# Kernel tuning notes

Measured on AMD Instinct MI355X. Metric: run time of the kernel, lower is better.

The kernel has to match this reference:

```python
import jax, jax.numpy as jnp
import numpy as np

BN_EPS = 1e-5
K2 = 9  # 3x3 kernel


def _conv3x3(x, w, b):
    # x: [B,C,H,W], w: [O,C,3,3] -> [B,O,H,W], stride 1, pad 1
    out = jax.lax.conv_general_dilated(
        x, w, window_strides=(1, 1), padding=((1, 1), (1, 1)),
        dimension_numbers=("NCHW", "OIHW", "NCHW"))
    return out + b[None, :, None, None]


def setup_inputs() -> dict:
    key = jax.random.key(0)
    ks = jax.random.split(key, 8)
    B, C, H, W = 8, 256, 64, 64
    O = 256
    x = jax.random.normal(ks[0], (B, C, H, W), dtype=jnp.float32)
    # offset/mask conv: small init so sampled offsets stay near the base grid
    w_off = jax.random.normal(ks[1], (3 * K2, C, 3, 3), dtype=jnp.float32) * 0.01
    b_off = jnp.zeros((3 * K2,), dtype=jnp.float32)
    weight = jax.random.normal(ks[2], (O, C, 3, 3), dtype=jnp.float32) * 0.02
    bias = jnp.zeros((O,), dtype=jnp.float32)
    gamma = jnp.ones((O,), dtype=jnp.float32)
    beta = jnp.zeros((O,), dtype=jnp.float32)
    run_mean = jax.random.normal(ks[3], (O,), dtype=jnp.float32) * 0.1
    run_var = jax.random.uniform(ks[4], (O,), dtype=jnp.float32) + 0.5
    return {"x": x, "w_off": w_off, "b_off": b_off, "weight": weight,
            "bias": bias, "gamma": gamma, "beta": beta,
            "run_mean": run_mean, "run_var": run_var}


def _deform_sample(img, py, px):
    # img: [C,H,W]; py, px: [K2,H,W] sampling coordinates.
    # Bilinear sample with zero padding outside (DCNv2 semantics:
    # out-of-bounds corners contribute zero).
    C, H, W = img.shape
    y0 = jnp.floor(py)
    x0 = jnp.floor(px)
    wy1 = py - y0  # frac weights for the 'high' corner
    wx1 = px - x0

    def gather(yi, xi):
        valid = (yi >= 0) & (yi < H) & (xi >= 0) & (xi < W)
        yc = jnp.clip(yi, 0, H - 1).astype(jnp.int32)
        xc = jnp.clip(xi, 0, W - 1).astype(jnp.int32)
        return img[:, yc, xc] * valid.astype(img.dtype)[None]  # [C,K2,H,W]

    v00 = gather(y0, x0)
    v01 = gather(y0, x0 + 1)
    v10 = gather(y0 + 1, x0)
    v11 = gather(y0 + 1, x0 + 1)
    return (v00 * ((1 - wy1) * (1 - wx1))[None]
            + v01 * ((1 - wy1) * wx1)[None]
            + v10 * (wy1 * (1 - wx1))[None]
            + v11 * (wy1 * wx1)[None])  # [C,K2,H,W]


def reference(x, w_off, b_off, weight, bias, gamma, beta, run_mean, run_var):
    B, C, H, W = x.shape
    O = weight.shape[0]
    # 1) offset / mask branch (standard 3x3 conv)
    om = _conv3x3(x, w_off, b_off)  # [B, 27, H, W]
    off_y = om[:, :K2]
    off_x = om[:, K2:2 * K2]
    mask = jax.nn.sigmoid(om[:, 2 * K2:])  # modulation, [B,9,H,W]
    # 2) base sampling grid for 3x3, stride 1, pad 1, dilation 1
    ky = jnp.repeat(jnp.arange(3), 3).astype(x.dtype)  # [9]
    kx = jnp.tile(jnp.arange(3), 3).astype(x.dtype)    # [9]
    hs = jnp.arange(H, dtype=x.dtype)
    ws = jnp.arange(W, dtype=x.dtype)
    base_y = hs[None, :, None] - 1.0 + ky[:, None, None]  # [9,H,1]
    base_x = ws[None, None, :] - 1.0 + kx[:, None, None]  # [9,1,W]
    py = base_y[None] + off_y  # [B,9,H,W]
    px = base_x[None] + off_x
    # 3) modulated deformable im2col (bilinear gather) per batch
    cols = jax.vmap(_deform_sample)(x, py, px)  # [B,C,9,H,W]
    cols = cols * mask[:, None]                 # apply modulation mask
    # 4) GEMM over (C, K2) + bias
    w3 = weight.reshape(O, C, K2)
    out = jnp.einsum("ock,bckhw->bohw", w3, cols) + bias[None, :, None, None]
    # 5) BatchNorm (eval mode, running stats) + ReLU
    inv = gamma / jnp.sqrt(run_var + BN_EPS)
    out = out * inv[None, :, None, None] + (beta - run_mean * inv)[None, :, None, None]
    return jax.nn.relu(out)
```

## Files before the change

kernel.cpp:

```cpp
#include <hip/hip_runtime.h>
#include <math.h>

#define H 64
#define W 64
#define C 256
#define O 256
#define CK 2304
#define NB 8
#define HWSZ 4096

typedef __attribute__((ext_vector_type(8))) short short8;
typedef __attribute__((ext_vector_type(4))) float floatx4;
typedef __attribute__((ext_vector_type(4))) unsigned uintx4;

#define FSWZ(n) ((((n) & 3) << 1) | (((n) >> 2) & 1))

__device__ __forceinline__ float lo2f(unsigned u) {
  return __builtin_bit_cast(float, u << 16);
}
__device__ __forceinline__ float hi2f(unsigned u) {
  return __builtin_bit_cast(float, u & 0xffff0000u);
}
__device__ __forceinline__ unsigned pk2bf(float v0, float v1) {
  unsigned a = __builtin_bit_cast(unsigned, v0);
  unsigned b = __builtin_bit_cast(unsigned, v1);
  return ((a + 0x8000u) >> 16) | ((b + 0x8000u) & 0xffff0000u);
}

__global__ __launch_bounds__(256) void prep_all(
    const float* __restrict__ x, const float* __restrict__ weight,
    const float* __restrict__ w_off, const float* __restrict__ bias,
    const float* __restrict__ gamma, const float* __restrict__ beta,
    const float* __restrict__ run_mean, const float* __restrict__ run_var,
    unsigned short* __restrict__ xt, unsigned short* __restrict__ wb,
    unsigned short* __restrict__ wob, float* __restrict__ invsh) {
  __shared__ unsigned tile[64 * 65];
  int bid = blockIdx.x;
  int tid = threadIdx.x;

  if (bid < 1024) {
    int b = bid & 7;
    int t = bid >> 3;
    int y = t >> 1;
    int cg = t & 1;
    const float* xb = x + ((size_t)b * C + cg * 128) * HWSZ + y * W;
#pragma unroll
    for (int it = 0; it < 4; ++it) {
      int e = tid + 256 * it;
      int xx4 = e & 15;
      int cp = e >> 4;
      floatx4 f0 = *reinterpret_cast<const floatx4*>(
          xb + (size_t)(2 * cp) * HWSZ + xx4 * 4);
      floatx4 f1 = *reinterpret_cast<const floatx4*>(
          xb + (size_t)(2 * cp + 1) * HWSZ + xx4 * 4);
#pragma unroll
      for (int k = 0; k < 4; ++k)
        tile[cp * 65 + xx4 * 4 + k] = pk2bf(f0[k], f1[k]);
    }
    __syncthreads();
    unsigned short* xo = xt + ((size_t)(b * 64 + y) << 14) + cg * 128;
#pragma unroll
    for (int it = 0; it < 4; ++it) {
      int e = tid + 256 * it;
      int cq = e & 15;
      int xx = e >> 4;
      unsigned u0 = tile[(cq * 4 + 0) * 65 + xx];
      unsigned u1 = tile[(cq * 4 + 1) * 65 + xx];
      unsigned u2 = tile[(cq * 4 + 2) * 65 + xx];
      unsigned u3 = tile[(cq * 4 + 3) * 65 + xx];
      uint4 v = {u0, u1, u2, u3};
      *reinterpret_cast<uint4*>(xo + (xx << 8) + (cq << 3)) = v;
    }
  } else if (bid < 1312) {
    int d0 = ((bid - 1024) * 256 + tid) * 8;
    int lane = (d0 >> 3) & 63;
    int mt = (d0 >> 9) & 15;
    int ks = d0 >> 13;
    int o = mt * 16 + (lane & 15);
    int kn0 = ks * 32 + (lane >> 4) * 8;
    int tap = kn0 >> 8;
    int c0 = kn0 & 255;
    const float* wsrc = weight + o * CK + c0 * 9 + tap;
    unsigned pk[4];
#pragma unroll
    for (int p = 0; p < 4; ++p)
      pk[p] = pk2bf(wsrc[(2 * p) * 9], wsrc[(2 * p + 1) * 9]);
    uint4 v = {pk[0], pk[1], pk[2], pk[3]};
    *reinterpret_cast<uint4*>(wb + d0) = v;
  } else if (bid < 1348) {
    int d0 = ((bid - 1312) * 256 + tid) * 8;
    int lane = (d0 >> 3) & 63;
    int mt = (d0 >> 9) & 1;
    int ks = d0 >> 10;
    int o = mt * 16 + (lane & 15);
    int kn0 = ks * 32 + (lane >> 4) * 8;
    int tap = kn0 >> 8;
    int c0 = kn0 & 255;
    uint4 v;
    if (o < 27) {
      const float* wsrc = w_off + o * CK + c0 * 9 + tap;
      unsigned pk[4];
#pragma unroll
      for (int p = 0; p < 4; ++p)
        pk[p] = pk2bf(wsrc[(2 * p) * 9], wsrc[(2 * p + 1) * 9]);
      v = (uint4){pk[0], pk[1], pk[2], pk[3]};
    } else {
      v = (uint4){0, 0, 0, 0};
    }
    *reinterpret_cast<uint4*>(wob + d0) = v;
  } else {
    int o = tid;
    float inv = gamma[o] * rsqrtf(run_var[o] + 1e-5f);
    invsh[o] = inv;
    invsh[O + o] = beta[o] + (bias[o] - run_mean[o]) * inv;
  }
}

__device__ __forceinline__ void sample_tap(
    int tap, const unsigned short* __restrict__ xtb, short* __restrict__ colbuf,
    const int* __restrict__ sbase, const float* __restrict__ s00,
    const float* __restrict__ s01, const float* __restrict__ s10,
    const float* __restrict__ s11, int sn, int scb) {
  int ei = tap * 64 + sn;
  int base = sbase[ei];
  float w00 = s00[ei], w01 = s01[ei], w10 = s10[ei], w11 = s11[ei];
  const unsigned short* p = xtb + base;
#pragma unroll
  for (int i = 0; i < 4; ++i) {
    int cbw = (i << 3) | scb;
    int co = cbw << 3;
    uintx4 u00 = *reinterpret_cast<const uintx4*>(p + co);
    uintx4 u01 = *reinterpret_cast<const uintx4*>(p + 256 + co);
    uintx4 u10 = *reinterpret_cast<const uintx4*>(p + 16384 + co);
    uintx4 u11 = *reinterpret_cast<const uintx4*>(p + 16640 + co);
    uintx4 res;
#pragma unroll
    for (int jd = 0; jd < 4; ++jd) {
      float v0 = fmaf(w00, lo2f(u00[jd]),
                 fmaf(w01, lo2f(u01[jd]),
                 fmaf(w10, lo2f(u10[jd]), w11 * lo2f(u11[jd]))));
      float v1 = fmaf(w00, hi2f(u00[jd]),
                 fmaf(w01, hi2f(u01[jd]),
                 fmaf(w10, hi2f(u10[jd]), w11 * hi2f(u11[jd]))));
      res[jd] = pk2bf(v0, v1);
    }
    int pos = (cbw ^ FSWZ(sn)) & 31;
    *reinterpret_cast<uintx4*>(&colbuf[(sn << 8) + (pos << 3)]) = res;
  }
}

__device__ __forceinline__ void mfma_tap(
    int tap, const unsigned short* __restrict__ wb,
    const short* __restrict__ colbuf, int wvid, int lane, int q, int lm,
    floatx4 (&acc)[2][4]) {
  __builtin_amdgcn_s_setprio(1);
#pragma unroll
  for (int s = 0; s < 8; ++s) {
    int ks = tap * 8 + s;
    short8 afrag[2];
#pragma unroll
    for (int a = 0; a < 2; ++a)
      afrag[a] = *reinterpret_cast<const short8*>(
          wb + (((ks * 16 + wvid * 2 + a) * 64 + lane) << 3));
    short8 bfrag[4];
#pragma unroll
    for (int u = 0; u < 4; ++u) {
      int nn = u * 16 + lm;
      int pos = ((s * 4 + q) ^ FSWZ(nn)) & 31;
      bfrag[u] = *reinterpret_cast<const short8*>(&colbuf[(nn << 8) + (pos << 3)]);
    }
#pragma unroll
    for (int a = 0; a < 2; ++a)
#pragma unroll
      for (int u = 0; u < 4; ++u)
        acc[a][u] = __builtin_amdgcn_mfma_f32_16x16x32_bf16(
            afrag[a], bfrag[u], acc[a][u], 0, 0, 0);
  }
  __builtin_amdgcn_s_setprio(0);
}

__global__ __launch_bounds__(512, 4) void deform_mfma_kernel(
    const unsigned short* __restrict__ xt, const unsigned short* __restrict__ wob,
    const float* __restrict__ b_off, const unsigned short* __restrict__ wb,
    const float* __restrict__ invsh, float* __restrict__ out) {
  __shared__ short cols[2][64 * 256];
  __shared__ int sbase[576];
  __shared__ float s00[576], s01[576], s10[576], s11[576];
  float* sm_om = reinterpret_cast<float*>(&cols[0][0]);

  int tid = threadIdx.x;
  int lane = tid & 63;
  int wvid = tid >> 6;
  int q = lane >> 4;
  int lm = lane & 15;
  int b = blockIdx.x;
  int h = blockIdx.y;
  const unsigned short* xtb = xt + ((size_t)b << 20);

  {
    int mt = wvid & 1;
    int nq = wvid >> 1;
    floatx4 a0 = (floatx4){0.f, 0.f, 0.f, 0.f};
    int pxn = nq * 16 + lm;
    for (int tap = 0; tap < 9; ++tap) {
      int yy = h - 1 + tap / 3;
      int xx = pxn - 1 + tap % 3;
      bool vv = (yy >= 0) && (yy < H) && (xx >= 0) && (xx < W);
      const unsigned short* bp =
          xtb + ((((yy & 63) << 6) + (xx & 63)) << 8) + q * 8;
#pragma unroll
      for (int s = 0; s < 8; ++s) {
        int ks = tap * 8 + s;
        short8 afrag = *reinterpret_cast<const short8*>(
            wob + (((ks * 2 + mt) * 64 + lane) << 3));
        short8 bfrag;
        if (vv)
          bfrag = *reinterpret_cast<const short8*>(bp + s * 32);
        else
          bfrag = (short8){0, 0, 0, 0, 0, 0, 0, 0};
        a0 = __builtin_amdgcn_mfma_f32_16x16x32_bf16(afrag, bfrag, a0, 0, 0, 0);
      }
    }
#pragma unroll
    for (int r = 0; r < 4; ++r) {
      int o = mt * 16 + q * 4 + r;
      if (o < 27) sm_om[o * 64 + pxn] = a0[r] + b_off[o];
    }
  }
  __syncthreads();

  for (int e = tid; e < 576; e += 512) {
    int n = e & 63;
    int k = e >> 6;
    float oy = sm_om[k * 64 + n];
    float ox = sm_om[(9 + k) * 64 + n];
    float mv = sm_om[(18 + k) * 64 + n];
    float m = 1.0f / (1.0f + __expf(-mv));
    float py = (float)(h - 1 + k / 3) + oy;
    float px = (float)(n - 1 + k % 3) + ox;
    float yf = floorf(py), xf = floorf(px);
    int y0 = (int)yf, x0 = (int)xf;
    float fy = py - yf, fx = px - xf;
    float r0, r1; int yl;
    if (y0 >= 0 && y0 <= H - 2)      { yl = y0;    r0 = 1.f - fy; r1 = fy;       }
    else if (y0 == -1)               { yl = 0;     r0 = fy;       r1 = 0.f;      }
    else if (y0 == H - 1)            { yl = H - 2; r0 = 0.f;      r1 = 1.f - fy; }
    else                             { yl = 0;     r0 = 0.f;      r1 = 0.f;      }
    float c0, c1; int xl;
    if (x0 >= 0 && x0 <= W - 2)      { xl = x0;    c0 = 1.f - fx; c1 = fx;       }
    else if (x0 == -1)               { xl = 0;     c0 = fx;       c1 = 0.f;      }
    else if (x0 == W - 1)            { xl = W - 2; c0 = 0.f;      c1 = 1.f - fx; }
    else                             { xl = 0;     c0 = 0.f;      c1 = 0.f;      }
    r0 *= m; r1 *= m;
    sbase[e] = ((yl << 6) + xl) << 8;
    s00[e] = r0 * c0; s01[e] = r0 * c1;
    s10[e] = r1 * c0; s11[e] = r1 * c1;
  }
  __syncthreads();

  floatx4 acc[2][4];
#pragma unroll
  for (int a = 0; a < 2; ++a)
#pragma unroll
    for (int u = 0; u < 4; ++u) acc[a][u] = (floatx4){0.f, 0.f, 0.f, 0.f};

  int sn = tid >> 3;
  int scb = tid & 7;

  sample_tap(0, xtb, cols[0], sbase, s00, s01, s10, s11, sn, scb);
  __syncthreads();

  for (int tap = 0; tap < 9; ++tap) {
    short* cur = cols[tap & 1];
    short* nxt = cols[(tap + 1) & 1];
    if (wvid & 1) {
      mfma_tap(tap, wb, cur, wvid, lane, q, lm, acc);
      if (tap < 8)
        sample_tap(tap + 1, xtb, nxt, sbase, s00, s01, s10, s11, sn, scb);
    } else {
      if (tap < 8)
        sample_tap(tap + 1, xtb, nxt, sbase, s00, s01, s10, s11, sn, scb);
      mfma_tap(tap, wb, cur, wvid, lane, q, lm, acc);
    }
    __syncthreads();
  }

#pragma unroll
  for (int a = 0; a < 2; ++a) {
#pragma unroll
    for (int u = 0; u < 4; ++u) {
      int nn = u * 16 + lm;
#pragma unroll
      for (int r = 0; r < 4; ++r) {
        int o = (wvid * 2 + a) * 16 + q * 4 + r;
        float v = fmaf(acc[a][u][r], invsh[o], invsh[O + o]);
        out[((size_t)(b * O + o)) * HWSZ + h * W + nn] = fmaxf(v, 0.0f);
      }
    }
  }
}

extern "C" void kernel_launch(void* const* d_in, const int* in_sizes, int n_in,
                              void* d_out, int out_size, void* d_ws, size_t ws_size,
                              hipStream_t stream) {
  const float* x        = (const float*)d_in[0];
  const float* w_off    = (const float*)d_in[1];
  const float* b_off    = (const float*)d_in[2];
  const float* weight   = (const float*)d_in[3];
  const float* bias     = (const float*)d_in[4];
  const float* gamma    = (const float*)d_in[5];
  const float* beta     = (const float*)d_in[6];
  const float* run_mean = (const float*)d_in[7];
  const float* run_var  = (const float*)d_in[8];
  float* out = (float*)d_out;

  char* ws = (char*)d_ws;
  unsigned short* xt = (unsigned short*)ws;
  unsigned short* wbf = (unsigned short*)(ws + 16777216);
  unsigned short* wob = (unsigned short*)(ws + 17956864);
  float* invsh = (float*)(ws + 18104320);

  prep_all<<<1349, 256, 0, stream>>>(x, weight, w_off, bias, gamma, beta,
                                     run_mean, run_var, xt, wbf, wob, invsh);
  {
    dim3 grid(NB, H);
    deform_mfma_kernel<<<grid, 512, 0, stream>>>(xt, wob, b_off, wbf, invsh, out);
  }
}
```

Baseline: 195.0 us.

## Interleave gather loads with half-tap MFMA work and use packed FMA

Splits each tap's bilinear sampling into two halves. Each half's global loads are issued before half of the MFMA work, so load latency hides behind matrix math in every wave. This replaces the earlier odd/even wave ordering, which only offset the two phases between waves. The bilinear blend now uses 2-wide float vector FMAs, which may map to packed FMA instructions. The cost is more live registers for in-flight loads, which could lower occupancy.

Result: slower. 208.8 us (+7.1%).

```diff
diff --git a/kernel.cpp b/kernel.cpp
--- a/kernel.cpp
+++ b/kernel.cpp
@@ -12,6 +12,7 @@
 typedef __attribute__((ext_vector_type(8))) short short8;
 typedef __attribute__((ext_vector_type(4))) float floatx4;
 typedef __attribute__((ext_vector_type(4))) unsigned uintx4;
+typedef __attribute__((ext_vector_type(2))) float f32x2;
 
 #define FSWZ(n) ((((n) & 3) << 1) | (((n) >> 2) & 1))
 
@@ -20,6 +21,9 @@
 }
 __device__ __forceinline__ float hi2f(unsigned u) {
   return __builtin_bit_cast(float, u & 0xffff0000u);
+}
+__device__ __forceinline__ f32x2 up2(unsigned u) {
+  return (f32x2){lo2f(u), hi2f(u)};
 }
 __device__ __forceinline__ unsigned pk2bf(float v0, float v1) {
   unsigned a = __builtin_bit_cast(unsigned, v0);
@@ -116,46 +120,49 @@
   }
 }
 
-__device__ __forceinline__ void sample_tap(
-    int tap, const unsigned short* __restrict__ xtb, short* __restrict__ colbuf,
-    const int* __restrict__ sbase, const float* __restrict__ s00,
-    const float* __restrict__ s01, const float* __restrict__ s10,
-    const float* __restrict__ s11, int sn, int scb) {
-  int ei = tap * 64 + sn;
-  int base = sbase[ei];
-  float w00 = s00[ei], w01 = s01[ei], w10 = s10[ei], w11 = s11[ei];
-  const unsigned short* p = xtb + base;
-#pragma unroll
-  for (int i = 0; i < 4; ++i) {
-    int cbw = (i << 3) | scb;
-    int co = cbw << 3;
-    uintx4 u00 = *reinterpret_cast<const uintx4*>(p + co);
-    uintx4 u01 = *reinterpret_cast<const uintx4*>(p + 256 + co);
-    uintx4 u10 = *reinterpret_cast<const uintx4*>(p + 16384 + co);
-    uintx4 u11 = *reinterpret_cast<const uintx4*>(p + 16640 + co);
+__device__ __forceinline__ void issue_half(
+    const unsigned short* __restrict__ p, int scb, int half,
+    uintx4 (&u00)[2], uintx4 (&u01)[2], uintx4 (&u10)[2], uintx4 (&u11)[2]) {
+#pragma unroll
+  for (int j = 0; j < 2; ++j) {
+    int co = (((half * 2 + j) << 3) | scb) << 3;
+    u00[j] = *reinterpret_cast<const uintx4*>(p + co);
+    u01[j] = *reinterpret_cast<const uintx4*>(p + 256 + co);
+    u10[j] = *reinterpret_cast<const uintx4*>(p + 16384 + co);
+    u11[j] = *reinterpret_cast<const uintx4*>(p + 16640 + co);
+  }
+}
+
+__device__ __forceinline__ void finish_half(
+    short* __restrict__ colbuf, int sn, int scb, int half,
+    f32x2 w00, f32x2 w01, f32x2 w10, f32x2 w11,
+    const uintx4 (&u00)[2], const uintx4 (&u01)[2],
+    const uintx4 (&u10)[2], const uintx4 (&u11)[2]) {
+#pragma unroll
+  for (int j = 0; j < 2; ++j) {
+    int cbw = ((half * 2 + j) << 3) | scb;
     uintx4 res;
 #pragma unroll
     for (int jd = 0; jd < 4; ++jd) {
-      float v0 = fmaf(w00, lo2f(u00[jd]),
-                 fmaf(w01, lo2f(u01[jd]),
-                 fmaf(w10, lo2f(u10[jd]), w11 * lo2f(u11[jd]))));
-      float v1 = fmaf(w00, hi2f(u00[jd]),
-                 fmaf(w01, hi2f(u01[jd]),
-                 fmaf(w10, hi2f(u10[jd]), w11 * hi2f(u11[jd]))));
-      res[jd] = pk2bf(v0, v1);
+      f32x2 a = up2(u00[j][jd]) * w00;
+      a = __builtin_elementwise_fma(up2(u01[j][jd]), w01, a);
+      a = __builtin_elementwise_fma(up2(u10[j][jd]), w10, a);
+      a = __builtin_elementwise_fma(up2(u11[j][jd]), w11, a);
+      res[jd] = pk2bf(a[0], a[1]);
     }
     int pos = (cbw ^ FSWZ(sn)) & 31;
     *reinterpret_cast<uintx4*>(&colbuf[(sn << 8) + (pos << 3)]) = res;
   }
 }
 
-__device__ __forceinline__ void mfma_tap(
-    int tap, const unsigned short* __restrict__ wb,
+__device__ __forceinline__ void mfma_half(
+    int tap, int half, const unsigned short* __restrict__ wb,
     const short* __restrict__ colbuf, int wvid, int lane, int q, int lm,
     floatx4 (&acc)[2][4]) {
   __builtin_amdgcn_s_setprio(1);
 #pragma unroll
-  for (int s = 0; s < 8; ++s) {
+  for (int s2 = 0; s2 < 4; ++s2) {
+    int s = half * 4 + s2;
     int ks = tap * 8 + s;
     short8 afrag[2];
 #pragma unroll
@@ -267,20 +274,40 @@
   int sn = tid >> 3;
   int scb = tid & 7;
 
-  sample_tap(0, xtb, cols[0], sbase, s00, s01, s10, s11, sn, scb);
+  {
+    const unsigned short* p = xtb + sbase[sn];
+    f32x2 w00 = (f32x2){s00[sn], s00[sn]};
+    f32x2 w01 = (f32x2){s01[sn], s01[sn]};
+    f32x2 w10 = (f32x2){s10[sn], s10[sn]};
+    f32x2 w11 = (f32x2){s11[sn], s11[sn]};
+    uintx4 u00[2], u01[2], u10[2], u11[2];
+    issue_half(p, scb, 0, u00, u01, u10, u11);
+    finish_half(cols[0], sn, scb, 0, w00, w01, w10, w11, u00, u01, u10, u11);
+    issue_half(p, scb, 1, u00, u01, u10, u11);
+    finish_half(cols[0], sn, scb, 1, w00, w01, w10, w11, u00, u01, u10, u11);
+  }
   __syncthreads();
 
   for (int tap = 0; tap < 9; ++tap) {
     short* cur = cols[tap & 1];
     short* nxt = cols[(tap + 1) & 1];
-    if (wvid & 1) {
-      mfma_tap(tap, wb, cur, wvid, lane, q, lm, acc);
-      if (tap < 8)
-        sample_tap(tap + 1, xtb, nxt, sbase, s00, s01, s10, s11, sn, scb);
+    if (tap < 8) {
+      int ei = (tap + 1) * 64 + sn;
+      const unsigned short* p = xtb + sbase[ei];
+      uintx4 u00[2], u01[2], u10[2], u11[2];
+      issue_half(p, scb, 0, u00, u01, u10, u11);
+      mfma_half(tap, 0, wb, cur, wvid, lane, q, lm, acc);
+      f32x2 w00 = (f32x2){s00[ei], s00[ei]};
+      f32x2 w01 = (f32x2){s01[ei], s01[ei]};
+      f32x2 w10 = (f32x2){s10[ei], s10[ei]};
+      f32x2 w11 = (f32x2){s11[ei], s11[ei]};
+      finish_half(nxt, sn, scb, 0, w00, w01, w10, w11, u00, u01, u10, u11);
+      issue_half(p, scb, 1, u00, u01, u10, u11);
+      mfma_half(tap, 1, wb, cur, wvid, lane, q, lm, acc);
+      finish_half(nxt, sn, scb, 1, w00, w01, w10, w11, u00, u01, u10, u11);
     } else {
-      if (tap < 8)
-        sample_tap(tap + 1, xtb, nxt, sbase, s00, s01, s10, s11, sn, scb);
-      mfma_tap(tap, wb, cur, wvid, lane, q, lm, acc);
+      mfma_half(tap, 0, wb, cur, wvid, lane, q, lm, acc);
+      mfma_half(tap, 1, wb, cur, wvid, lane, q, lm, acc);
     }
     __syncthreads();
   }
```
